# Kernel tuning notes

Hardware: AMD Instinct MI355X
Metric: run time of the kernel (lower is better)

The kernel has to match this reference:

```python
import jax, jax.numpy as jnp
import numpy as np
from jax import lax

CUTOFF = 0.25
SIGMA = 1.0
RADIUS = 4  # skimage/scipy default truncate=4.0 -> radius = round(4.0*sigma)


def _gauss_kernel(sigma=SIGMA, radius=RADIUS):
    x = np.arange(-radius, radius + 1, dtype=np.float32)
    k = np.exp(-0.5 * (x / sigma) ** 2)
    return jnp.asarray(k / k.sum())


def _blur_axis(x, axis, kernel):
    r = (kernel.shape[0] - 1) // 2
    pad = [(0, 0)] * x.ndim
    pad[axis] = (r, r)
    xp = jnp.pad(x, pad, mode='edge')  # scipy mode='nearest'
    out = jnp.zeros_like(x)
    for i in range(kernel.shape[0]):  # fixed small tap loop (9 taps)
        out = out + kernel[i] * lax.slice_in_dim(xp, i, i + x.shape[axis], axis=axis)
    return out


def gaussian_smoothing_4d(x):
    # skimage.filters.gaussian on a 4D array smooths over ALL axes (B, C, H, W)
    k = _gauss_kernel().astype(x.dtype)
    for ax in range(4):
        x = _blur_axis(x, ax, k)
    return x


def dht_2d(x):
    # real(FFT(x)) - imag(FFT(flip(x)))
    return (jnp.fft.fftn(x, axes=(2, 3)).real
            - jnp.fft.fftn(jnp.flip(x, axis=(2, 3)), axes=(2, 3)).imag).astype(x.dtype)


def _neg_k(a):
    # X_H(-k): flip both spatial mode axes, then roll by 1 (DC stays put)
    return jnp.roll(jnp.flip(a, axis=(-2, -1)), shift=(1, 1), axis=(-2, -1))


def compl_mul2d(x1, x2):
    x1n, x2n = _neg_k(x1), _neg_k(x2)
    e = lambda a, b: jnp.einsum('bixy,ioxy->boxy', a, b)
    return 0.5 * (e(x1, x2) - e(x1n, x2n) + e(x1, x2n) + e(x1n, x2))


def setup_inputs() -> dict:
    key = jax.random.key(0)
    k1, k2 = jax.random.split(key)
    B, Cin, Cout, H, W, M1, M2 = 16, 64, 64, 128, 128, 20, 20
    x = jax.random.normal(k1, (B, Cin, H, W), dtype=jnp.float32)
    scale = 1.0 / (Cin * Cout)
    w1 = scale * jax.random.uniform(k2, (Cin, Cout, M1, M2), dtype=jnp.float32)
    return {'x': x, 'w1': w1}


def reference(x, w1):
    B, _, H, W = x.shape
    Cout, M1, M2 = w1.shape[1], w1.shape[2], w1.shape[3]
    x_ht = dht_2d(x)
    out_ht = jnp.zeros((B, Cout, H, W), dtype=x.dtype)
    out_ht = out_ht.at[:, :, :M1, :M2].set(
        compl_mul2d(x_ht[:, :, :M1, :M2], w1))
    # inverse DHT = DHT / (H*W)
    y = dht_2d(out_ht) / (H * W)
    y = gaussian_smoothing_4d(y)
    # low-pass mask along last dim only (as in the original)
    freqs = jnp.fft.fftfreq(W)
    mask = (jnp.abs(freqs) <= CUTOFF).astype(y.dtype)
    return y * mask
```

## Files before the change

kernel.cpp:

```cpp
#include <hip/hip_runtime.h>


#define TWO_PI 6.283185307179586f
#define THETA (TWO_PI / 128.0f)

__device__ __forceinline__ void gauss9(float* g) {
  float s = 0.f;
#pragma unroll
  for (int t = 0; t < 9; ++t) { float d = (float)(t - 4); g[t] = expf(-0.5f * d * d); s += g[t]; }
  float inv = 1.f / s;
#pragma unroll
  for (int t = 0; t < 9; ++t) g[t] *= inv;
}

__global__ void __launch_bounds__(256, 4) kBig(
    const float* __restrict__ x, const float* __restrict__ w1,
    float* __restrict__ X1, float* __restrict__ wbT,
    float* __restrict__ L2g, float* __restrict__ RB2g) {
  __shared__ float lds[10240];
  int tid = threadIdx.x;
  int blk = blockIdx.x;

  if (blk < 448) {
    int c = blk / 7, chunk = blk % 7;
    int m0 = chunk * 64;
    int mw = 400 - m0; if (mw > 64) mw = 64;
    for (int t = tid; t < 4096; t += 256) {
      int o = t >> 6, mm = t & 63;
      lds[o * 69 + mm] = (mm < mw) ? w1[(c * 64 + o) * 400 + m0 + mm] : 0.f;
    }
    __syncthreads();
    float g[9]; gauss9(g);
    for (int t = tid; t < 4096; t += 256) {
      int mm = t >> 6, o = t & 63;
      if (mm >= mw) continue;
      float acc = 0.f;
#pragma unroll
      for (int tp = 0; tp < 9; ++tp) {
        int oc = o - 4 + tp; oc = oc < 0 ? 0 : (oc > 63 ? 63 : oc);
        acc += g[tp] * lds[oc * 69 + mm];
      }
      wbT[(c * 400 + m0 + mm) * 64 + o] = acc;
    }
    return;
  }
  if (blk == 448) {
    for (int i = tid; i < 5376; i += 256) {
      int u = i / 42, t = i - u * 42;
      int A = (t < 21) ? t : t - 21;
      float a = (float)((u * A) & 127) * THETA;
      lds[u * 44 + t] = (t < 21) ? cosf(a) : sinf(a);
    }
    __syncthreads();
    float g[9]; gauss9(g);
    for (int i = tid; i < 5376; i += 256) {
      int u = i / 42, t = i - u * 42;
      float acc = 0.f;
#pragma unroll
      for (int tp = 0; tp < 9; ++tp) {
        int uc = u - 4 + tp; uc = uc < 0 ? 0 : (uc > 127 ? 127 : uc);
        acc += g[tp] * lds[uc * 44 + t];
      }
      L2g[t * 128 + u] = acc;
      bool keep = (u <= 32) || (u >= 96);
      RB2g[t * 128 + u] = keep ? acc : 0.f;
    }
    return;
  }

  int bc = blk - 449;
  const float* xb = x + (long)bc * 16384;

  for (int i = tid; i < 2560; i += 256) {
    int n2 = i / 20, k2 = i - n2 * 20;
    float s, c;
    sincosf((float)((k2 * n2) & 127) * THETA, &s, &c);
    lds[n2 * 40 + k2] = c;
    lds[n2 * 40 + 20 + k2] = s;
  }

  int rg = tid & 31, cg = tid >> 5;
  int r0 = rg * 4, c0 = cg * 5;
  float acc[4][5];
#pragma unroll
  for (int i = 0; i < 4; ++i)
#pragma unroll
    for (int j = 0; j < 5; ++j) acc[i][j] = 0.f;

  float* xs = lds + 5120;
  for (int ch = 0; ch < 4; ++ch) {
    __syncthreads();
    for (int t = tid; t < 1024; t += 256) {
      int n2l = t & 31, n1g = t >> 5;
      const float* gp = xb + n1g * 512 + ch * 32 + n2l;
      float4 v = make_float4(gp[0], gp[128], gp[256], gp[384]);
      *(float4*)&xs[n2l * 132 + n1g * 4] = v;
    }
    __syncthreads();
#pragma unroll 4
    for (int k = 0; k < 32; ++k) {
      float4 av = *(const float4*)&xs[k * 132 + r0];
      const float* tr = lds + (ch * 32 + k) * 40 + c0;
      float avv[4] = {av.x, av.y, av.z, av.w};
      float bvv[5] = {tr[0], tr[1], tr[2], tr[3], tr[4]};
#pragma unroll
      for (int i = 0; i < 4; ++i)
#pragma unroll
        for (int j = 0; j < 5; ++j) acc[i][j] += avv[i] * bvv[j];
    }
  }
  __syncthreads();
  for (int i = tid; i < 2560; i += 256) {
    int k1 = i >> 7, t = i & 127;
    float s, c;
    sincosf((float)((k1 * t) & 127) * THETA, &s, &c);
    lds[k1 * 128 + (t ^ ((k1 & 7) << 2))] = c;
    lds[(20 + k1) * 128 + (t ^ (((20 + k1) & 7) << 2))] = s;
  }
#pragma unroll
  for (int j = 0; j < 5; ++j) {
    int col = c0 + j;
    int k2 = (col < 20) ? col : col - 20;
    int part = (col < 20) ? 0 : 128;
    int m = (k2 & 7) << 2;
    *(float4*)&lds[5120 + k2 * 256 + ((part + r0) ^ m)] =
        make_float4(acc[0][j], acc[1][j], acc[2][j], acc[3][j]);
  }
  __syncthreads();
  if (tid < 200) {
    int k1 = tid / 10, k2 = (tid % 10) * 2;
    int mc = (k1 & 7) << 2, ms = ((20 + k1) & 7) << 2;
    int m0 = (k2 & 7) << 2, m1 = ((k2 + 1) & 7) << 2;
    const float* tgc = lds + k1 * 128;
    const float* tgs = lds + (20 + k1) * 128;
    const float* p0 = lds + 5120 + k2 * 256;
    const float* p1 = lds + 5120 + (k2 + 1) * 256;
    float Ac0 = 0.f, As0 = 0.f, Bc0 = 0.f, Bs0 = 0.f;
    float Ac1 = 0.f, As1 = 0.f, Bc1 = 0.f, Bs1 = 0.f;
    for (int t = 0; t < 128; t += 4) {
      float4 tc = *(const float4*)(tgc + (t ^ mc));
      float4 ts = *(const float4*)(tgs + (t ^ ms));
      float4 pc0 = *(const float4*)(p0 + (t ^ m0));
      float4 ps0 = *(const float4*)(p0 + 128 + (t ^ m0));
      float4 pc1 = *(const float4*)(p1 + (t ^ m1));
      float4 ps1 = *(const float4*)(p1 + 128 + (t ^ m1));
      Ac0 += tc.x*pc0.x + tc.y*pc0.y + tc.z*pc0.z + tc.w*pc0.w;
      As0 += ts.x*pc0.x + ts.y*pc0.y + ts.z*pc0.z + ts.w*pc0.w;
      Bc0 += tc.x*ps0.x + tc.y*ps0.y + tc.z*ps0.z + tc.w*ps0.w;
      Bs0 += ts.x*ps0.x + ts.y*ps0.y + ts.z*ps0.z + ts.w*ps0.w;
      Ac1 += tc.x*pc1.x + tc.y*pc1.y + tc.z*pc1.z + tc.w*pc1.w;
      As1 += ts.x*pc1.x + ts.y*pc1.y + ts.z*pc1.z + ts.w*pc1.w;
      Bc1 += tc.x*ps1.x + tc.y*ps1.y + tc.z*ps1.z + tc.w*ps1.w;
      Bs1 += ts.x*ps1.x + ts.y*ps1.y + ts.z*ps1.z + ts.w*ps1.w;
    }
    float sa, ca, sb, cb;
    sincosf(THETA * (float)(k1 + k2), &sa, &ca);
    sincosf(THETA * (float)(k1 + k2 + 1), &sb, &cb);
    X1[(k1 * 20 + k2) * 1024 + bc] = (Ac0 - Bs0) * (1.f - sa) - (As0 + Bc0) * ca;
    X1[(k1 * 20 + k2 + 1) * 1024 + bc] = (Ac1 - Bs1) * (1.f - sb) - (As1 + Bc1) * cb;
  }
}

__global__ void k3_mix(const float* __restrict__ X1, const float* __restrict__ wbT,
                       float* __restrict__ O) {
  __shared__ float Xp[16][64], Xm[16][64];
  int m = blockIdx.x;
  int i = m / 20, j = m - i * 20;
  int nm = ((20 - i) % 20) * 20 + ((20 - j) % 20);
  int tid = threadIdx.x;
  const float sc = 0.5f / 16384.0f;
  float g[9]; gauss9(g);
  {
    int bl = tid >> 6, c = tid & 63;
#pragma unroll
    for (int it = 0; it < 4; ++it) {
      int b = bl * 4 + it;
      float sa = 0.f, sn = 0.f;
#pragma unroll
      for (int tp = 0; tp < 9; ++tp) {
        int bb = b - 4 + tp; bb = bb < 0 ? 0 : (bb > 15 ? 15 : bb);
        sa += g[tp] * X1[m * 1024 + bb * 64 + c];
        sn += g[tp] * X1[nm * 1024 + bb * 64 + c];
      }
      Xp[b][c] = (sa + sn) * sc; Xm[b][c] = (sa - sn) * sc;
    }
  }
  __syncthreads();
  int o = tid & 63, bq = tid >> 6;
  float acc[4] = {0.f, 0.f, 0.f, 0.f};
#pragma unroll 4
  for (int c = 0; c < 64; ++c) {
    float wp = wbT[(c * 400 + m) * 64 + o];
    float wm = wbT[(c * 400 + nm) * 64 + o];
#pragma unroll
    for (int k = 0; k < 4; ++k)
      acc[k] += Xp[bq * 4 + k][c] * wp + Xm[bq * 4 + k][c] * wm;
  }
#pragma unroll
  for (int k = 0; k < 4; ++k)
    O[((bq * 4 + k) * 64 + o) * 400 + m] = acc[k];
}

__global__ void __launch_bounds__(256) k5b_final(const float* __restrict__ O,
                                                 const float* __restrict__ L2g,
                                                 const float* __restrict__ RB2g,
                                                 float* __restrict__ out) {
  __shared__ float Os[400];
  __shared__ float Rs[42 * 128];
  int bo = blockIdx.x, tid = threadIdx.x;
  for (int t = tid; t < 400; t += 256) Os[t] = O[bo * 400 + t];
  __syncthreads();
  const float4* Bc4 = (const float4*)RB2g;
  const float4* Bs4 = (const float4*)(RB2g + 21 * 128);
  {
    int rg = tid & 7;
    int vqIdx = tid >> 3;
    int vq = (vqIdx < 9) ? vqIdx : vqIdx + 15;
    if (rg < 7 && vqIdx < 17) {
      int r0 = rg * 6;
      float4 a[6];
#pragma unroll
      for (int q = 0; q < 6; ++q) a[q] = make_float4(0.f, 0.f, 0.f, 0.f);
      for (int k2 = 0; k2 <= 20; ++k2) {
        float4 bc4 = Bc4[k2 * 32 + vq];
        float4 bs4 = Bs4[k2 * 32 + vq];
#pragma unroll
        for (int q = 0; q < 6; ++q) {
          int r = r0 + q;
          bool isS = (r >= 21);
          int A = isS ? (r - 21) : r;
          if (k2 < 20 && A < 20) {
            float ov = Os[A * 20 + k2];
            const float4 b = isS ? bs4 : bc4;
            float s = isS ? -ov : ov;
            a[q].x += s * b.x; a[q].y += s * b.y; a[q].z += s * b.z; a[q].w += s * b.w;
          }
          if (k2 >= 1 && A >= 1) {
            float ov = Os[(A - 1) * 20 + (k2 - 1)];
            const float4 b = isS ? bc4 : bs4;
            a[q].x -= ov * b.x; a[q].y -= ov * b.y; a[q].z -= ov * b.z; a[q].w -= ov * b.w;
          }
        }
      }
#pragma unroll
      for (int q = 0; q < 6; ++q)
        *(float4*)&Rs[(r0 + q) * 128 + vq * 4] = a[q];
    }
  }
  __syncthreads();
  long base = (long)bo * 16384;
  {
    int half = tid >> 7;
    int uu = (tid >> 3) & 15;  int u0 = uu * 8;
    int vv = tid & 7;          int v0 = half ? (96 + vv * 4) : vv * 4;
    float acc[8][4];
#pragma unroll
    for (int a = 0; a < 8; ++a)
#pragma unroll
      for (int b = 0; b < 4; ++b) acc[a][b] = 0.f;
    for (int r = 0; r < 42; ++r) {
      float4 a0 = *(const float4*)(L2g + r * 128 + u0);
      float4 a1 = *(const float4*)(L2g + r * 128 + u0 + 4);
      float4 b0 = *(const float4*)&Rs[r * 128 + v0];
      float av[8] = {a0.x, a0.y, a0.z, a0.w, a1.x, a1.y, a1.z, a1.w};
      float bv[4] = {b0.x, b0.y, b0.z, b0.w};
#pragma unroll
      for (int a = 0; a < 8; ++a)
#pragma unroll
        for (int b = 0; b < 4; ++b) acc[a][b] += av[a] * bv[b];
    }
#pragma unroll
    for (int a = 0; a < 8; ++a)
      *(float4*)&out[base + (u0 + a) * 128 + v0] =
          make_float4(acc[a][0], acc[a][1], acc[a][2], acc[a][3]);
  }
  if (tid < 128) {
    float d = 0.f;
    for (int r = 0; r < 42; ++r) d += L2g[r * 128 + tid] * Rs[r * 128 + 32];
    out[base + tid * 128 + 32] = d;
  }
  float4 z4 = make_float4(0.f, 0.f, 0.f, 0.f);
  for (int jj = tid; jj < 2048; jj += 256) {
    int u = jj >> 4, s = jj & 15;
    long p = base + (long)u * 128;
    if (s == 15) { out[p + 33] = 0.f; out[p + 34] = 0.f; out[p + 35] = 0.f; }
    else *(float4*)&out[p + 36 + 4 * s] = z4;
  }
}

extern "C" void kernel_launch(void* const* d_in, const int* in_sizes, int n_in,
                              void* d_out, int out_size, void* d_ws, size_t ws_size,
                              hipStream_t stream) {
  const float* x = (const float*)d_in[0];
  const float* w1 = (const float*)d_in[1];
  float* out = (float*)d_out;
  float* ws = (float*)d_ws;

  float* X1 = ws;
  float* O = X1 + 409600;
  float* wbT = O + 409600;
  float* L2g = wbT + 1638400;
  float* RB2g = L2g + 5376;

  hipLaunchKernelGGL(kBig, dim3(1473), dim3(256), 0, stream,
                     x, w1, X1, wbT, L2g, RB2g);
  hipLaunchKernelGGL(k3_mix, dim3(400), dim3(256), 0, stream, X1, wbT, O);
  hipLaunchKernelGGL(k5b_final, dim3(1024), dim3(256), 0, stream, O, L2g, RB2g, out);
}
```

Baseline: 192.4 us.

## Exploit cos/sin symmetry to halve first DFT stage and reorder block dispatch

The first-axis DFT now folds x[n] and x[128-n] into even and odd sums, so cosine terms use the sum and sine terms use the difference. This halves the multiply-accumulate work and the twiddle table size of the per-image transform stage. Block indices are also rearranged so the 1024 per-image transform blocks run first and the weight-blur and table blocks come after. Each thread group now reads one of two staging buffers, and the middle sample n=64 gets a special-case tail step.

```diff
diff --git a/kernel.cpp b/kernel.cpp
--- a/kernel.cpp
+++ b/kernel.cpp
@@ -21,8 +21,32 @@
   int tid = threadIdx.x;
   int blk = blockIdx.x;
 
-  if (blk < 448) {
-    int c = blk / 7, chunk = blk % 7;
+  if (blk >= 1024) {
+    if (blk == 1472) {
+      for (int i = tid; i < 5376; i += 256) {
+        int u = i / 42, t = i - u * 42;
+        int A = (t < 21) ? t : t - 21;
+        float a = (float)((u * A) & 127) * THETA;
+        lds[u * 44 + t] = (t < 21) ? cosf(a) : sinf(a);
+      }
+      __syncthreads();
+      float g[9]; gauss9(g);
+      for (int i = tid; i < 5376; i += 256) {
+        int u = i / 42, t = i - u * 42;
+        float acc = 0.f;
+#pragma unroll
+        for (int tp = 0; tp < 9; ++tp) {
+          int uc = u - 4 + tp; uc = uc < 0 ? 0 : (uc > 127 ? 127 : uc);
+          acc += g[tp] * lds[uc * 44 + t];
+        }
+        L2g[t * 128 + u] = acc;
+        bool keep = (u <= 32) || (u >= 96);
+        RB2g[t * 128 + u] = keep ? acc : 0.f;
+      }
+      return;
+    }
+    int bb = blk - 1024;
+    int c = bb / 7, chunk = bb % 7;
     int m0 = chunk * 64;
     int mw = 400 - m0; if (mw > 64) mw = 64;
     for (int t = tid; t < 4096; t += 256) {
@@ -44,39 +68,16 @@
     }
     return;
   }
-  if (blk == 448) {
-    for (int i = tid; i < 5376; i += 256) {
-      int u = i / 42, t = i - u * 42;
-      int A = (t < 21) ? t : t - 21;
-      float a = (float)((u * A) & 127) * THETA;
-      lds[u * 44 + t] = (t < 21) ? cosf(a) : sinf(a);
-    }
-    __syncthreads();
-    float g[9]; gauss9(g);
-    for (int i = tid; i < 5376; i += 256) {
-      int u = i / 42, t = i - u * 42;
-      float acc = 0.f;
-#pragma unroll
-      for (int tp = 0; tp < 9; ++tp) {
-        int uc = u - 4 + tp; uc = uc < 0 ? 0 : (uc > 127 ? 127 : uc);
-        acc += g[tp] * lds[uc * 44 + t];
-      }
-      L2g[t * 128 + u] = acc;
-      bool keep = (u <= 32) || (u >= 96);
-      RB2g[t * 128 + u] = keep ? acc : 0.f;
-    }
-    return;
-  }
-
-  int bc = blk - 449;
+
+  int bc = blk;
   const float* xb = x + (long)bc * 16384;
 
-  for (int i = tid; i < 2560; i += 256) {
-    int n2 = i / 20, k2 = i - n2 * 20;
+  for (int i = tid; i < 2600; i += 256) {
+    int n2 = i / 40, col = i - n2 * 40;
+    int k2 = (col < 20) ? col : col - 20;
     float s, c;
     sincosf((float)((k2 * n2) & 127) * THETA, &s, &c);
-    lds[n2 * 40 + k2] = c;
-    lds[n2 * 40 + 20 + k2] = s;
+    lds[i] = (col < 20) ? c : s;
   }
 
   int rg = tid & 31, cg = tid >> 5;
@@ -87,26 +88,57 @@
 #pragma unroll
     for (int j = 0; j < 5; ++j) acc[i][j] = 0.f;
 
-  float* xs = lds + 5120;
+  float* xsP = lds + 2600;
+  float* xsM = lds + 4844;
+  const float* xsrc = (cg < 4) ? xsP : xsM;
+
   for (int ch = 0; ch < 4; ++ch) {
     __syncthreads();
-    for (int t = tid; t < 1024; t += 256) {
-      int n2l = t & 31, n1g = t >> 5;
-      const float* gp = xb + n1g * 512 + ch * 32 + n2l;
+#pragma unroll
+    for (int it = 0; it < 2; ++it) {
+      int t = tid + it * 256;
+      int n2l = t & 15, n1g = t >> 4;
+      int base = ch * 16 + n2l;
+      const float* gp = xb + n1g * 512 + base;
+      float a0 = gp[0], a1 = gp[128], a2 = gp[256], a3 = gp[384];
+      float b0 = 0.f, b1 = 0.f, b2 = 0.f, b3 = 0.f;
+      if (base != 0) {
+        const float* gm = xb + n1g * 512 + (128 - base);
+        b0 = gm[0]; b1 = gm[128]; b2 = gm[256]; b3 = gm[384];
+      }
+      *(float4*)&xsP[n2l * 132 + n1g * 4] =
+          make_float4(a0 + b0, a1 + b1, a2 + b2, a3 + b3);
+      *(float4*)&xsM[n2l * 132 + n1g * 4] =
+          make_float4(a0 - b0, a1 - b1, a2 - b2, a3 - b3);
+    }
+    if (ch == 3 && tid < 32) {
+      int n1g = tid;
+      const float* gp = xb + n1g * 512 + 64;
       float4 v = make_float4(gp[0], gp[128], gp[256], gp[384]);
-      *(float4*)&xs[n2l * 132 + n1g * 4] = v;
+      *(float4*)&xsP[16 * 132 + n1g * 4] = v;
+      *(float4*)&xsM[16 * 132 + n1g * 4] = v;
     }
     __syncthreads();
 #pragma unroll 4
-    for (int k = 0; k < 32; ++k) {
-      float4 av = *(const float4*)&xs[k * 132 + r0];
-      const float* tr = lds + (ch * 32 + k) * 40 + c0;
+    for (int k = 0; k < 16; ++k) {
+      float4 av = *(const float4*)&xsrc[k * 132 + r0];
+      const float* tr = lds + (ch * 16 + k) * 40 + c0;
+      float bv[5] = {tr[0], tr[1], tr[2], tr[3], tr[4]};
       float avv[4] = {av.x, av.y, av.z, av.w};
-      float bvv[5] = {tr[0], tr[1], tr[2], tr[3], tr[4]};
 #pragma unroll
       for (int i = 0; i < 4; ++i)
 #pragma unroll
-        for (int j = 0; j < 5; ++j) acc[i][j] += avv[i] * bvv[j];
+        for (int j = 0; j < 5; ++j) acc[i][j] += avv[i] * bv[j];
+    }
+    if (ch == 3) {
+      float4 av = *(const float4*)&xsrc[16 * 132 + r0];
+      const float* tr = lds + 64 * 40 + c0;
+      float bv[5] = {tr[0], tr[1], tr[2], tr[3], tr[4]};
+      float avv[4] = {av.x, av.y, av.z, av.w};
+#pragma unroll
+      for (int i = 0; i < 4; ++i)
+#pragma unroll
+        for (int j = 0; j < 5; ++j) acc[i][j] += avv[i] * bv[j];
     }
   }
   __syncthreads();
```

Measured after the change: 183.5 us. -4.7%, faster.
